# Optimization experiments

Measured on AMD Instinct MI355X. Metric: run time of the kernel, lower is better.

Reference implementation:

```python
import jax, jax.numpy as jnp
import numpy as np

BLOCK_SIZE = 16
NVFP4_LEVELS = np.array([0.0, 0.5, 1.0, 1.5, 2.0, 3.0, 4.0, 6.0], dtype=np.float32)


def quantize_to_nvfp4(x, block_size=BLOCK_SIZE):
    """NVFP4 fake-quant: per-16-element block, scale = amax/6, round |x| to nearest level."""
    levels = jnp.asarray(NVFP4_LEVELS, dtype=x.dtype)
    orig_shape = x.shape
    xf = x.reshape(-1, block_size)                                   # [nblk, 16]
    amax = jnp.clip(jnp.max(jnp.abs(xf), axis=-1, keepdims=True), 1e-12)
    scale = amax / 6.0                                               # [nblk, 1]
    x_norm = jnp.abs(xf) / scale                                     # in [0, 6]
    idx = jnp.argmin(jnp.abs(x_norm[..., None] - levels), axis=-1)   # nearest level (first on ties, like torch)
    x_q = jnp.sign(xf) * levels[idx] * scale
    return x_q.reshape(orig_shape)


def _magnitude_mask_2_4(w):
    # keep 2 largest-|.| of every group of 4 along in_features (row-wise 2:4)
    out_f, in_f = w.shape
    a = jnp.abs(w).reshape(out_f, in_f // 4, 4)
    thr = jnp.sort(a, axis=-1)[..., 2:3]          # 2nd-largest magnitude in group
    mask = (a >= thr).reshape(out_f, in_f)
    return mask.astype(w.dtype)


def setup_inputs() -> dict:
    key = jax.random.key(0)
    k_x, k_w, k_s, k_a, k_b, k_bias = jax.random.split(key, 6)
    B, S, IN_F, OUT_F, RANK = 2, 2048, 4096, 4096, 32
    x = jax.random.normal(k_x, (B, S, IN_F), dtype=jnp.float32)
    smooth_scale = jax.random.uniform(k_s, (IN_F,), dtype=jnp.float32, minval=0.5, maxval=2.0)
    # realistic calibrated weight: 2:4 magnitude-sparse then NVFP4 fake-quantized
    w = jax.random.normal(k_w, (OUT_F, IN_F), dtype=jnp.float32) * 0.02
    w_sparse = w * _magnitude_mask_2_4(w)
    w_quantized = quantize_to_nvfp4(w_sparse)
    lora_a = jax.random.normal(k_a, (RANK, IN_F), dtype=jnp.float32) * 0.02
    lora_b = jax.random.normal(k_b, (OUT_F, RANK), dtype=jnp.float32) * 0.02
    bias = jax.random.normal(k_bias, (OUT_F,), dtype=jnp.float32)
    return {"x": x, "smooth_scale": smooth_scale, "w_quantized": w_quantized,
            "lora_a": lora_a, "lora_b": lora_b, "bias": bias}


def reference(x, smooth_scale, w_quantized, lora_a, lora_b, bias):
    # x: [B, S, IN], smooth_scale: [IN], w_quantized: [OUT, IN]
    x_smoothed = x * smooth_scale                                    # SmoothQuant activation scaling
    x_q = quantize_to_nvfp4(x_smoothed, BLOCK_SIZE)                  # block fake-quant of activations
    base_out = jnp.einsum('bsi,oi->bso', x_q, w_quantized)           # 2:4-sparse quantized matmul
    svd_out = jnp.einsum('bsr,or->bso',
                         jnp.einsum('bsi,ri->bsr', x_smoothed, lora_a), lora_b)  # low-rank correction
    return base_out + svd_out + bias
```

## Files before the change

kernel.cpp:

```cpp
#include <hip/hip_runtime.h>
#include <hip/hip_bf16.h>
#include <stdint.h>

typedef __attribute__((ext_vector_type(8)))  __bf16 bf16x8;
typedef __attribute__((ext_vector_type(4)))  float  f32x4;

#define KP 4224

__device__ inline void async_copy16(const void* g, void* l) {
  __builtin_amdgcn_global_load_lds((const __attribute__((address_space(1))) void*)g,
                                   (__attribute__((address_space(3))) void*)l, 16, 0, 0);
}

__global__ __launch_bounds__(256) void fused_quant_lora_kernel(
    const float* __restrict__ x, const float* __restrict__ ss,
    const float* __restrict__ la, __bf16* __restrict__ Ab,
    float* __restrict__ Tp) {
  __shared__ float red[4][16][32];
  int tid  = threadIdx.x;
  int m0   = blockIdx.x << 4;
  int by   = blockIdx.y;

  {
    int row = m0 + (tid >> 4);
    int cb0 = tid & 15;
#pragma unroll
    for (int i = 0; i < 4; i++) {
      int col = (by << 10) + ((cb0 + (i << 4)) << 4);
      const float4* xp = (const float4*)(x + ((size_t)row << 12) + col);
      const float4* sp = (const float4*)(ss + col);
      float xs[16];
#pragma unroll
      for (int j = 0; j < 4; j++) {
        float4 xv = xp[j]; float4 sv = sp[j];
        xs[4*j+0] = xv.x * sv.x; xs[4*j+1] = xv.y * sv.y;
        xs[4*j+2] = xv.z * sv.z; xs[4*j+3] = xv.w * sv.w;
      }
      float amax = 0.f;
#pragma unroll
      for (int j = 0; j < 16; j++) amax = fmaxf(amax, fabsf(xs[j]));
      amax = fmaxf(amax, 1e-12f);
      float scale = amax / 6.0f;
      bf16x8 o0, o1;
#pragma unroll
      for (int j = 0; j < 16; j++) {
        float a  = fabsf(xs[j]);
        float xn = a / scale;
        float bestd = xn;
        float lvl   = 0.f;
        const float L[7] = {0.5f, 1.f, 1.5f, 2.f, 3.f, 4.f, 6.f};
#pragma unroll
        for (int l = 0; l < 7; l++) {
          float d = fabsf(xn - L[l]);
          if (d < bestd) { bestd = d; lvl = L[l]; }
        }
        float mag = lvl * scale;
        float q = (xs[j] > 0.f) ? mag : ((xs[j] < 0.f) ? -mag : 0.f);
        if (j < 8) o0[j] = (__bf16)q; else o1[j-8] = (__bf16)q;
      }
      __bf16* dst = Ab + (size_t)row * KP + col;
      *(bf16x8*)dst = o0;
      *(bf16x8*)(dst + 8) = o1;
    }
  }

  {
    int wave = tid >> 6, lane = tid & 63;
    int lrow = lane & 15, kg = lane >> 4;
    int kbase = (by << 10) + (wave << 8);
    f32x4 acc0 = {0.f,0.f,0.f,0.f}, acc1 = {0.f,0.f,0.f,0.f};
    const float* xrow = x + ((size_t)(m0 + lrow) << 12);
    const float* a0   = la + ((size_t)lrow << 12);
    const float* a1   = a0 + (16 << 12);
#pragma unroll
    for (int k0 = 0; k0 < 256; k0 += 32) {
      int kk = kbase + k0 + (kg << 3);
      float xv[8], sv[8], v0[8], v1[8];
      *(float4*)&xv[0] = *(const float4*)(xrow + kk);
      *(float4*)&xv[4] = *(const float4*)(xrow + kk + 4);
      *(float4*)&sv[0] = *(const float4*)(ss + kk);
      *(float4*)&sv[4] = *(const float4*)(ss + kk + 4);
      *(float4*)&v0[0] = *(const float4*)(a0 + kk);
      *(float4*)&v0[4] = *(const float4*)(a0 + kk + 4);
      *(float4*)&v1[0] = *(const float4*)(a1 + kk);
      *(float4*)&v1[4] = *(const float4*)(a1 + kk + 4);
      bf16x8 af, b0, b1;
#pragma unroll
      for (int j = 0; j < 8; j++) {
        af[j] = (__bf16)(xv[j] * sv[j]);
        b0[j] = (__bf16)v0[j];
        b1[j] = (__bf16)v1[j];
      }
      acc0 = __builtin_amdgcn_mfma_f32_16x16x32_bf16(af, b0, acc0, 0, 0, 0);
      acc1 = __builtin_amdgcn_mfma_f32_16x16x32_bf16(af, b1, acc1, 0, 0, 0);
    }
#pragma unroll
    for (int r = 0; r < 4; r++) {
      red[wave][kg*4 + r][lrow]      = acc0[r];
      red[wave][kg*4 + r][16 + lrow] = acc1[r];
    }
    __syncthreads();
    for (int o = tid; o < 512; o += 256) {
      int rr = o >> 5, cc = o & 31;
      float s = red[0][rr][cc] + red[1][rr][cc] + red[2][rr][cc] + red[3][rr][cc];
      Tp[((size_t)by * 4096 + m0 + rr) * 32 + cc] = s;
    }
  }
}

__global__ __launch_bounds__(256) void wconv_fix_kernel(const float* __restrict__ w,
                                                        const float* __restrict__ lb,
                                                        const float* __restrict__ Tp,
                                                        __bf16* __restrict__ Bb,
                                                        __bf16* __restrict__ Ab) {
  int b = blockIdx.x;
  if (b < 8448) {
    int id  = b * 256 + threadIdx.x;
    int row = id / 528;
    int g   = id - row * 528;
    bf16x8 v;
    if (g < 512) {
      const float4* wp = (const float4*)(w + ((size_t)row << 12) + (g << 3));
      float4 a = wp[0], bb = wp[1];
      v[0]=(__bf16)a.x;  v[1]=(__bf16)a.y;  v[2]=(__bf16)a.z;  v[3]=(__bf16)a.w;
      v[4]=(__bf16)bb.x; v[5]=(__bf16)bb.y; v[6]=(__bf16)bb.z; v[7]=(__bf16)bb.w;
    } else if (g < 516) {
      const float* p = lb + (size_t)row * 32 + ((g - 512) << 3);
#pragma unroll
      for (int j = 0; j < 8; j++) v[j] = (__bf16)p[j];
    } else {
#pragma unroll
      for (int j = 0; j < 8; j++) v[j] = (__bf16)0.f;
    }
    *(bf16x8*)(Bb + (size_t)row * KP + ((size_t)g << 3)) = v;
  } else {
    int id  = (b - 8448) * 256 + threadIdx.x;
    int row = id >> 5, cc = id & 31;
    float s = 0.f;
#pragma unroll
    for (int kc = 0; kc < 4; kc++)
      s += Tp[((size_t)kc * 4096 + row) * 32 + cc];
    __bf16* dst = Ab + (size_t)row * KP + 4096;
    dst[cc]      = (__bf16)s;
    dst[32 + cc] = (__bf16)0.f;
    dst[64 + cc] = (__bf16)0.f;
    dst[96 + cc] = (__bf16)0.f;
  }
}

#define GBAR() __builtin_amdgcn_s_barrier()
#define PRI1() __builtin_amdgcn_s_setprio(1)
#define PRI0() __builtin_amdgcn_s_setprio(0)
#define WVM(n) asm volatile("s_waitcnt vmcnt(" #n ")" ::: "memory")

#define STG(srcb, dstb, bb, h, t) do {                                         \
    const __bf16* _s = (srcb) + (size_t)(h) * (128 * (size_t)KP)               \
                              + ((size_t)(t) << 6);                            \
    char* _d = (dstb) + ((bb) << 15) + ((h) << 14);                            \
    async_copy16(_s, _d);                                                      \
    async_copy16(_s + 32, _d + 1024);                                          \
  } while (0)

#define RDA(p, MFB) do { _Pragma("unroll")                                     \
  for (int u = 0; u < 8; u++)                                                  \
    Afr[u] = *(const bf16x8*)((p) + ((((MFB)*2) + u) << 10)); } while (0)

#define RDB(p, NFB) do { _Pragma("unroll")                                     \
  for (int u = 0; u < 4; u++)                                                  \
    Bfr[(NFB)*2 + u] = *(const bf16x8*)((p) + ((((NFB)*2) + u) << 10)); } while (0)

#define MM(MFB, NFB) do {                                                      \
  _Pragma("unroll") for (int mf = 0; mf < 4; mf++)                             \
  _Pragma("unroll") for (int nf = 0; nf < 2; nf++)                             \
  _Pragma("unroll") for (int ks = 0; ks < 2; ks++)                             \
    acc[(MFB)+mf][(NFB)+nf] = __builtin_amdgcn_mfma_f32_16x16x32_bf16(         \
        Afr[mf*2+ks], Bfr[((NFB)+nf)*2+ks], acc[(MFB)+mf][(NFB)+nf], 0, 0, 0); \
  } while (0)

__global__ __launch_bounds__(512, 2) void gemm_kernel(const __bf16* __restrict__ A,
                                                      const __bf16* __restrict__ B,
                                                      const float* __restrict__ bias,
                                                      float* __restrict__ C) {
  extern __shared__ char lds[];
  const int tid  = threadIdx.x;
  const int w    = tid >> 6, lane = tid & 63;
  const int ln15 = lane & 15, kg = lane >> 4;
  const int wm   = w >> 2, wn = w & 3;
  const int bid  = blockIdx.x;
  const int sbid = ((bid & 7) << 5) | (bid >> 3);
  const int bm   = sbid >> 4, bn = sbid & 15;
  const size_t m0 = (size_t)bm << 8, n0 = (size_t)bn << 8;

  const int rr = (w << 4) + (lane >> 2);
  const int kk = ((lane & 3) ^ (((lane >> 5) & 1) << 1)) << 3;
  const __bf16* aS = A + (m0 + rr) * (size_t)KP + kk;
  const __bf16* bS = B + (n0 + rr) * (size_t)KP + kk;
  char* dA = lds + (w << 11);
  char* dB = lds + 65536 + (w << 11);

  int inner = (ln15 << 6) + (kg << 4);
  inner ^= (ln15 & 8) << 2;
  const char* pA0 = lds + (wm << 14) + inner;
  const char* pA1 = pA0 + 32768;
  const char* pB0 = lds + 65536 + (wn << 13) + inner;
  const char* pB1 = pB0 + 32768;

  bf16x8 Afr[8], Bfr[8];
  f32x4 acc[8][4];
#pragma unroll
  for (int i = 0; i < 8; i++)
#pragma unroll
    for (int j = 0; j < 4; j++) acc[i][j] = (f32x4){0.f, 0.f, 0.f, 0.f};

  STG(bS, dB, 0, 0, 0); STG(bS, dB, 0, 1, 0);
  STG(aS, dA, 0, 0, 0); STG(aS, dA, 0, 1, 0);
  STG(bS, dB, 1, 0, 1); STG(bS, dB, 1, 1, 1);
  WVM(4);
  GBAR();

#pragma unroll 1
  for (int i = 0; i < 32; i++) {
    const int t1 = 2*i + 1, t2 = 2*i + 2, t3 = 2*i + 3;
    RDA(pA0, 0); RDB(pB0, 0); STG(aS, dA, 1, 0, t1);
    GBAR(); PRI1(); MM(0, 0); PRI0(); GBAR();
    RDB(pB0, 2); STG(aS, dA, 1, 1, t1);
    GBAR(); PRI1(); MM(0, 2); PRI0(); GBAR();
    RDA(pA0, 4); STG(bS, dB, 0, 0, t2);
    GBAR(); PRI1(); MM(4, 0); PRI0(); GBAR();
    STG(bS, dB, 0, 1, t2);
    GBAR(); PRI1(); MM(4, 2); PRI0(); WVM(4); GBAR();
    RDA(pA1, 0); RDB(pB1, 0); STG(aS, dA, 0, 0, t2);
    GBAR(); PRI1(); MM(0, 0); PRI0(); GBAR();
    RDB(pB1, 2); STG(aS, dA, 0, 1, t2);
    GBAR(); PRI1(); MM(0, 2); PRI0(); GBAR();
    RDA(pA1, 4); STG(bS, dB, 1, 0, t3);
    GBAR(); PRI1(); MM(4, 0); PRI0(); GBAR();
    STG(bS, dB, 1, 1, t3);
    GBAR(); PRI1(); MM(4, 2); PRI0(); WVM(4); GBAR();
  }

  RDA(pA0, 0); RDB(pB0, 0); STG(aS, dA, 1, 0, 65);
  GBAR(); PRI1(); MM(0, 0); PRI0(); GBAR();
  RDB(pB0, 2); STG(aS, dA, 1, 1, 65);
  GBAR(); PRI1(); MM(0, 2); PRI0(); GBAR();
  RDA(pA0, 4);
  GBAR(); PRI1(); MM(4, 0); PRI0(); GBAR();
  GBAR(); PRI1(); MM(4, 2); PRI0(); WVM(0); GBAR();
  RDA(pA1, 0); RDB(pB1, 0);
  GBAR(); PRI1(); MM(0, 0); PRI0(); GBAR();
  RDB(pB1, 2);
  GBAR(); PRI1(); MM(0, 2); PRI0(); GBAR();
  RDA(pA1, 4);
  GBAR(); PRI1(); MM(4, 0); PRI0(); GBAR();
  GBAR(); PRI1(); MM(4, 2); PRI0(); GBAR();

  const int    colb = (int)n0 + (wn << 6) + ln15;
  const size_t rowb = m0 + ((size_t)wm << 7) + (kg << 2);
#pragma unroll
  for (int nf = 0; nf < 4; nf++) {
    const int col = colb + (nf << 4);
    const float bv = bias[col];
#pragma unroll
    for (int mf = 0; mf < 8; mf++) {
      const size_t r0 = rowb + ((size_t)mf << 4);
#pragma unroll
      for (int q = 0; q < 4; q++)
        C[(r0 + q) * 4096 + col] = acc[mf][nf][q] + bv;
    }
  }
}

extern "C" void kernel_launch(void* const* d_in, const int* in_sizes, int n_in,
                              void* d_out, int out_size, void* d_ws, size_t ws_size,
                              hipStream_t stream) {
  const float* x    = (const float*)d_in[0];
  const float* ss   = (const float*)d_in[1];
  const float* w    = (const float*)d_in[2];
  const float* la   = (const float*)d_in[3];
  const float* lb   = (const float*)d_in[4];
  const float* bias = (const float*)d_in[5];
  float* out = (float*)d_out;

  __bf16* Ab = (__bf16*)d_ws;
  __bf16* Bb = Ab + (size_t)4096 * KP;
  float* Tp = out;

  static bool s_attr = false;
  if (!s_attr) {
    hipFuncSetAttribute((const void*)gemm_kernel,
                        hipFuncAttributeMaxDynamicSharedMemorySize, 131072);
    s_attr = true;
  }

  fused_quant_lora_kernel<<<dim3(256, 4), 256, 0, stream>>>(x, ss, la, Ab, Tp);
  wconv_fix_kernel<<<8960, 256, 0, stream>>>(w, lb, Tp, Bb, Ab);
  gemm_kernel<<<256, 512, 131072, stream>>>(Ab, Bb, bias, out);
}
```

Before: 311.0 us.

## Double-buffer GEMM register fragments, closed-form FP4 rounding, finer quant grid

The GEMM main loop now keeps two sets of A and B register fragments and loads the next set from LDS while MFMAs consume the current one. This removes the barrier pair that used to sit around each LDS read. The quant kernel replaces the 7-level nearest-search loop with a closed-form ceil expression plus a few comparisons. It also doubles the grid in the K dimension (8 column chunks instead of 4), with the partial-sum reduction updated to match. The risks are higher register pressure from the extra fragments, and tie-breaking in the closed-form rounding that may differ from argmin's first-on-ties rule.

```diff
diff --git a/kernel.cpp b/kernel.cpp
--- a/kernel.cpp
+++ b/kernel.cpp
@@ -25,8 +25,8 @@
     int row = m0 + (tid >> 4);
     int cb0 = tid & 15;
 #pragma unroll
-    for (int i = 0; i < 4; i++) {
-      int col = (by << 10) + ((cb0 + (i << 4)) << 4);
+    for (int i = 0; i < 2; i++) {
+      int col = (by << 9) + ((cb0 + (i << 4)) << 4);
       const float4* xp = (const float4*)(x + ((size_t)row << 12) + col);
       const float4* sp = (const float4*)(ss + col);
       float xs[16];
@@ -46,13 +46,12 @@
       for (int j = 0; j < 16; j++) {
         float a  = fabsf(xs[j]);
         float xn = a / scale;
-        float bestd = xn;
-        float lvl   = 0.f;
-        const float L[7] = {0.5f, 1.f, 1.5f, 2.f, 3.f, 4.f, 6.f};
-#pragma unroll
-        for (int l = 0; l < 7; l++) {
-          float d = fabsf(xn - L[l]);
-          if (d < bestd) { bestd = d; lvl = L[l]; }
+        float lvl;
+        if (xn < 2.25f) {
+          lvl = 0.5f * __builtin_ceilf(__builtin_fmaf(2.0f, xn, -0.5f));
+        } else {
+          lvl = (xn <= 2.5f) ? 2.0f : (xn <= 3.5f) ? 3.0f
+              : (xn <= 5.0f) ? 4.0f : 6.0f;
         }
         float mag = lvl * scale;
         float q = (xs[j] > 0.f) ? mag : ((xs[j] < 0.f) ? -mag : 0.f);
@@ -67,13 +66,13 @@
   {
     int wave = tid >> 6, lane = tid & 63;
     int lrow = lane & 15, kg = lane >> 4;
-    int kbase = (by << 10) + (wave << 8);
+    int kbase = (by << 9) + (wave << 7);
     f32x4 acc0 = {0.f,0.f,0.f,0.f}, acc1 = {0.f,0.f,0.f,0.f};
     const float* xrow = x + ((size_t)(m0 + lrow) << 12);
     const float* a0   = la + ((size_t)lrow << 12);
     const float* a1   = a0 + (16 << 12);
 #pragma unroll
-    for (int k0 = 0; k0 < 256; k0 += 32) {
+    for (int k0 = 0; k0 < 128; k0 += 32) {
       int kk = kbase + k0 + (kg << 3);
       float xv[8], sv[8], v0[8], v1[8];
       *(float4*)&xv[0] = *(const float4*)(xrow + kk);
@@ -138,7 +137,7 @@
     int row = id >> 5, cc = id & 31;
     float s = 0.f;
 #pragma unroll
-    for (int kc = 0; kc < 4; kc++)
+    for (int kc = 0; kc < 8; kc++)
       s += Tp[((size_t)kc * 4096 + row) * 32 + cc];
     __bf16* dst = Ab + (size_t)row * KP + 4096;
     dst[cc]      = (__bf16)s;
@@ -161,20 +160,20 @@
     async_copy16(_s + 32, _d + 1024);                                          \
   } while (0)
 
-#define RDA(p, MFB) do { _Pragma("unroll")                                     \
+#define LD8(dst, p, off) do { _Pragma("unroll")                                \
   for (int u = 0; u < 8; u++)                                                  \
-    Afr[u] = *(const bf16x8*)((p) + ((((MFB)*2) + u) << 10)); } while (0)
-
-#define RDB(p, NFB) do { _Pragma("unroll")                                     \
+    dst[u] = *(const bf16x8*)((p) + (((off) + u) << 10)); } while (0)
+
+#define LD4(dst, p, off) do { _Pragma("unroll")                                \
   for (int u = 0; u < 4; u++)                                                  \
-    Bfr[(NFB)*2 + u] = *(const bf16x8*)((p) + ((((NFB)*2) + u) << 10)); } while (0)
-
-#define MM(MFB, NFB) do {                                                      \
+    dst[u] = *(const bf16x8*)((p) + (((off) + u) << 10)); } while (0)
+
+#define MMQ(Ar, Br, MFB, NFB) do {                                             \
   _Pragma("unroll") for (int mf = 0; mf < 4; mf++)                             \
   _Pragma("unroll") for (int nf = 0; nf < 2; nf++)                             \
   _Pragma("unroll") for (int ks = 0; ks < 2; ks++)                             \
     acc[(MFB)+mf][(NFB)+nf] = __builtin_amdgcn_mfma_f32_16x16x32_bf16(         \
-        Afr[mf*2+ks], Bfr[((NFB)+nf)*2+ks], acc[(MFB)+mf][(NFB)+nf], 0, 0, 0); \
+        Ar[mf*2+ks], Br[nf*2+ks], acc[(MFB)+mf][(NFB)+nf], 0, 0, 0);           \
   } while (0)
 
 __global__ __launch_bounds__(512, 2) void gemm_kernel(const __bf16* __restrict__ A,
@@ -205,7 +204,7 @@
   const char* pB0 = lds + 65536 + (wn << 13) + inner;
   const char* pB1 = pB0 + 32768;
 
-  bf16x8 Afr[8], Bfr[8];
+  bf16x8 Ax[8], Ay[8], Bg0[4], Bg1[4];
   f32x4 acc[8][4];
 #pragma unroll
   for (int i = 0; i < 8; i++)
@@ -217,42 +216,65 @@
   STG(bS, dB, 1, 0, 1); STG(bS, dB, 1, 1, 1);
   WVM(4);
   GBAR();
+  LD8(Ax, pA0, 0); LD4(Bg0, pB0, 0);
 
 #pragma unroll 1
   for (int i = 0; i < 32; i++) {
     const int t1 = 2*i + 1, t2 = 2*i + 2, t3 = 2*i + 3;
-    RDA(pA0, 0); RDB(pB0, 0); STG(aS, dA, 1, 0, t1);
-    GBAR(); PRI1(); MM(0, 0); PRI0(); GBAR();
-    RDB(pB0, 2); STG(aS, dA, 1, 1, t1);
-    GBAR(); PRI1(); MM(0, 2); PRI0(); GBAR();
-    RDA(pA0, 4); STG(bS, dB, 0, 0, t2);
-    GBAR(); PRI1(); MM(4, 0); PRI0(); GBAR();
+    GBAR();
+    STG(aS, dA, 1, 0, t1);
+    LD8(Ay, pA0, 8); LD4(Bg1, pB0, 4);
+    PRI1(); MMQ(Ax, Bg0, 0, 0); PRI0();
+    GBAR();
+    STG(aS, dA, 1, 1, t1);
+    PRI1(); MMQ(Ax, Bg1, 0, 2); PRI0();
+    GBAR();
+    STG(bS, dB, 0, 0, t2);
+    PRI1(); MMQ(Ay, Bg0, 4, 0); PRI0();
+    WVM(2);
+    GBAR();
     STG(bS, dB, 0, 1, t2);
-    GBAR(); PRI1(); MM(4, 2); PRI0(); WVM(4); GBAR();
-    RDA(pA1, 0); RDB(pB1, 0); STG(aS, dA, 0, 0, t2);
-    GBAR(); PRI1(); MM(0, 0); PRI0(); GBAR();
-    RDB(pB1, 2); STG(aS, dA, 0, 1, t2);
-    GBAR(); PRI1(); MM(0, 2); PRI0(); GBAR();
-    RDA(pA1, 4); STG(bS, dB, 1, 0, t3);
-    GBAR(); PRI1(); MM(4, 0); PRI0(); GBAR();
+    LD8(Ax, pA1, 0); LD4(Bg0, pB1, 0);
+    PRI1(); MMQ(Ay, Bg1, 4, 2); PRI0();
+    GBAR();
+    STG(aS, dA, 0, 0, t2);
+    LD8(Ay, pA1, 8); LD4(Bg1, pB1, 4);
+    PRI1(); MMQ(Ax, Bg0, 0, 0); PRI0();
+    GBAR();
+    STG(aS, dA, 0, 1, t2);
+    PRI1(); MMQ(Ax, Bg1, 0, 2); PRI0();
+    GBAR();
+    STG(bS, dB, 1, 0, t3);
+    PRI1(); MMQ(Ay, Bg0, 4, 0); PRI0();
+    WVM(2);
+    GBAR();
     STG(bS, dB, 1, 1, t3);
-    GBAR(); PRI1(); MM(4, 2); PRI0(); WVM(4); GBAR();
-  }
-
-  RDA(pA0, 0); RDB(pB0, 0); STG(aS, dA, 1, 0, 65);
-  GBAR(); PRI1(); MM(0, 0); PRI0(); GBAR();
-  RDB(pB0, 2); STG(aS, dA, 1, 1, 65);
-  GBAR(); PRI1(); MM(0, 2); PRI0(); GBAR();
-  RDA(pA0, 4);
-  GBAR(); PRI1(); MM(4, 0); PRI0(); GBAR();
-  GBAR(); PRI1(); MM(4, 2); PRI0(); WVM(0); GBAR();
-  RDA(pA1, 0); RDB(pB1, 0);
-  GBAR(); PRI1(); MM(0, 0); PRI0(); GBAR();
-  RDB(pB1, 2);
-  GBAR(); PRI1(); MM(0, 2); PRI0(); GBAR();
-  RDA(pA1, 4);
-  GBAR(); PRI1(); MM(4, 0); PRI0(); GBAR();
-  GBAR(); PRI1(); MM(4, 2); PRI0(); GBAR();
+    LD8(Ax, pA0, 0); LD4(Bg0, pB0, 0);
+    PRI1(); MMQ(Ay, Bg1, 4, 2); PRI0();
+  }
+
+  GBAR();
+  STG(aS, dA, 1, 0, 65);
+  LD8(Ay, pA0, 8); LD4(Bg1, pB0, 4);
+  PRI1(); MMQ(Ax, Bg0, 0, 0); PRI0();
+  GBAR();
+  STG(aS, dA, 1, 1, 65);
+  PRI1(); MMQ(Ax, Bg1, 0, 2); PRI0();
+  GBAR();
+  PRI1(); MMQ(Ay, Bg0, 4, 0); PRI0();
+  WVM(0);
+  GBAR();
+  LD8(Ax, pA1, 0); LD4(Bg0, pB1, 0);
+  PRI1(); MMQ(Ay, Bg1, 4, 2); PRI0();
+  GBAR();
+  LD8(Ay, pA1, 8); LD4(Bg1, pB1, 4);
+  PRI1(); MMQ(Ax, Bg0, 0, 0); PRI0();
+  GBAR();
+  PRI1(); MMQ(Ax, Bg1, 0, 2); PRI0();
+  GBAR();
+  PRI1(); MMQ(Ay, Bg0, 4, 0); PRI0();
+  GBAR();
+  PRI1(); MMQ(Ay, Bg1, 4, 2); PRI0();
 
   const int    colb = (int)n0 + (wn << 6) + ln15;
   const size_t rowb = m0 + ((size_t)wm << 7) + (kg << 2);
@@ -292,7 +314,7 @@
     s_attr = true;
   }
 
-  fused_quant_lora_kernel<<<dim3(256, 4), 256, 0, stream>>>(x, ss, la, Ab, Tp);
+  fused_quant_lora_kernel<<<dim3(256, 8), 256, 0, stream>>>(x, ss, la, Ab, Tp);
   wconv_fix_kernel<<<8960, 256, 0, stream>>>(w, lb, Tp, Bb, Ab);
   gemm_kernel<<<256, 512, 131072, stream>>>(Ab, Bb, bias, out);
 }
```

After: 310.1 us. Within noise of the previous version (-0.3%).
